# Optimization experiments

Measured on AMD Instinct MI355X. Metric: run time of the kernel, lower is better.

The kernel has to match this reference:

```python
import jax, jax.numpy as jnp
import numpy as np

N_ROWS = 5000  # hard-coded loop bound in the source
N_FEAT = 20    # hard-coded x size in the source


def setup_inputs() -> dict:
    key = jax.random.key(0)
    kA, kb, kx = jax.random.split(key, 3)
    A = jax.random.normal(kA, (N_ROWS, N_FEAT), dtype=jnp.float32)
    b = jax.random.normal(kb, (N_ROWS,), dtype=jnp.float32)
    # nn.Parameter initialized as uniform(low=1, high=13, size=20)
    x = 1.0 + 12.0 * jax.random.uniform(kx, (N_FEAT,), dtype=jnp.float32)
    return {"A": A, "b": b, "x": x}


def reference(A, b, x):
    # Original: loss = sum_i ||A[i,:] @ x - b||^2, where the scalar A[i]@x
    # broadcasts against the full vector b each iteration.
    # Vectorized: s = A @ x (shape [N_ROWS]); residual r[i,j] = s[i] - b[j].
    s = A @ x                                   # [5000]
    r = s[:, None] - b[None, :]                  # [5000, 5000] broadcasted residual
    return jnp.sum(r * r)
```

## Files before the change

kernel.cpp:

```cpp
#include <hip/hip_runtime.h>
#include <hip/hip_bf16.h>


#define N_ROWS 5000
#define N_FEAT 20
#define NBLK   20
#define BLKSZ  256

__device__ __forceinline__ double wave_reduce_sum(double v) {
    #pragma unroll
    for (int off = 32; off > 0; off >>= 1)
        v += __shfl_down(v, off, 64);
    return v;
}

__global__ __launch_bounds__(BLKSZ) void lsq_partial_kernel(
        const float* __restrict__ A, const float* __restrict__ b,
        const float* __restrict__ x, double* __restrict__ ws) {
    __shared__ float xs[N_FEAT];
    if (threadIdx.x < N_FEAT) xs[threadIdx.x] = x[threadIdx.x];
    __syncthreads();

    double s1 = 0.0, s2 = 0.0, b1 = 0.0, b2 = 0.0;
    for (int i = blockIdx.x * BLKSZ + threadIdx.x; i < N_ROWS;
         i += NBLK * BLKSZ) {
        const float* __restrict__ row = A + (long)i * N_FEAT;
        float s = 0.0f;
        #pragma unroll
        for (int k = 0; k < N_FEAT; ++k) s += row[k] * xs[k];
        s1 += (double)s;
        s2 += (double)s * (double)s;
        float bv = b[i];
        b1 += (double)bv;
        b2 += (double)bv * (double)bv;
    }

    s1 = wave_reduce_sum(s1);
    s2 = wave_reduce_sum(s2);
    b1 = wave_reduce_sum(b1);
    b2 = wave_reduce_sum(b2);

    __shared__ double red[4][4];
    int lane = threadIdx.x & 63;
    int wave = threadIdx.x >> 6;
    if (lane == 0) {
        red[wave][0] = s1; red[wave][1] = s2;
        red[wave][2] = b1; red[wave][3] = b2;
    }
    __syncthreads();
    if (threadIdx.x == 0) {
        double t0 = 0, t1 = 0, t2 = 0, t3 = 0;
        #pragma unroll
        for (int w = 0; w < 4; ++w) {
            t0 += red[w][0]; t1 += red[w][1];
            t2 += red[w][2]; t3 += red[w][3];
        }
        double* p = ws + 4 * blockIdx.x;
        p[0] = t0; p[1] = t1; p[2] = t2; p[3] = t3;
    }
}

__global__ __launch_bounds__(64) void lsq_finalize_kernel(
        const double* __restrict__ ws, float* __restrict__ out) {
    double s1 = 0, s2 = 0, b1 = 0, b2 = 0;
    if (threadIdx.x < NBLK) {
        const double* p = ws + 4 * threadIdx.x;
        s1 = p[0]; s2 = p[1]; b1 = p[2]; b2 = p[3];
    }
    s1 = wave_reduce_sum(s1);
    s2 = wave_reduce_sum(s2);
    b1 = wave_reduce_sum(b1);
    b2 = wave_reduce_sum(b2);
    if (threadIdx.x == 0) {
        double n = (double)N_ROWS;
        out[0] = (float)(n * s2 - 2.0 * s1 * b1 + n * b2);
    }
}

extern "C" void kernel_launch(void* const* d_in, const int* in_sizes, int n_in,
                              void* d_out, int out_size, void* d_ws, size_t ws_size,
                              hipStream_t stream) {
    const float* A = (const float*)d_in[0];
    const float* b = (const float*)d_in[1];
    const float* x = (const float*)d_in[2];
    float* out = (float*)d_out;
    double* ws = (double*)d_ws;

    lsq_partial_kernel<<<NBLK, BLKSZ, 0, stream>>>(A, b, x, ws);
    lsq_finalize_kernel<<<1, 64, 0, stream>>>(ws, out);
}
```

Before: 59.74 us.

## Fuse partial and finalize reductions into one single-block kernel with float4 loads

Replaces the two-kernel reduction (20 blocks plus a finalize launch) with one 1024-thread block that computes the row dot products, reduces them, and writes the final scalar. Rows are read as five float4 loads and x is held in registers. This removes a kernel launch and the workspace round trip, but puts the whole 400KB read on a single CU, which may limit memory bandwidth.

```diff
diff --git a/kernel.cpp b/kernel.cpp
--- a/kernel.cpp
+++ b/kernel.cpp
@@ -4,8 +4,8 @@
 
 #define N_ROWS 5000
 #define N_FEAT 20
-#define NBLK   20
-#define BLKSZ  256
+#define BLKSZ  1024
+#define NWAVES (BLKSZ / 64)
 
 __device__ __forceinline__ double wave_reduce_sum(double v) {
     #pragma unroll
@@ -14,23 +14,32 @@
     return v;
 }
 
-__global__ __launch_bounds__(BLKSZ) void lsq_partial_kernel(
+__global__ __launch_bounds__(BLKSZ) void lsq_fused_kernel(
         const float* __restrict__ A, const float* __restrict__ b,
-        const float* __restrict__ x, double* __restrict__ ws) {
+        const float* __restrict__ x, float* __restrict__ out) {
     __shared__ float xs[N_FEAT];
     if (threadIdx.x < N_FEAT) xs[threadIdx.x] = x[threadIdx.x];
     __syncthreads();
 
+    float x0 = xs[0],  x1 = xs[1],  x2 = xs[2],  x3 = xs[3],  x4 = xs[4];
+    float x5 = xs[5],  x6 = xs[6],  x7 = xs[7],  x8 = xs[8],  x9 = xs[9];
+    float x10 = xs[10], x11 = xs[11], x12 = xs[12], x13 = xs[13], x14 = xs[14];
+    float x15 = xs[15], x16 = xs[16], x17 = xs[17], x18 = xs[18], x19 = xs[19];
+
     double s1 = 0.0, s2 = 0.0, b1 = 0.0, b2 = 0.0;
-    for (int i = blockIdx.x * BLKSZ + threadIdx.x; i < N_ROWS;
-         i += NBLK * BLKSZ) {
-        const float* __restrict__ row = A + (long)i * N_FEAT;
-        float s = 0.0f;
-        #pragma unroll
-        for (int k = 0; k < N_FEAT; ++k) s += row[k] * xs[k];
+    for (int i = threadIdx.x; i < N_ROWS; i += BLKSZ) {
+        const float4* __restrict__ row = (const float4*)(A + (long)i * N_FEAT);
+        float4 r0 = row[0], r1 = row[1], r2 = row[2], r3 = row[3], r4 = row[4];
+        float bv = b[i];
+
+        float s = r0.x * x0  + r0.y * x1  + r0.z * x2  + r0.w * x3
+                + r1.x * x4  + r1.y * x5  + r1.z * x6  + r1.w * x7
+                + r2.x * x8  + r2.y * x9  + r2.z * x10 + r2.w * x11
+                + r3.x * x12 + r3.y * x13 + r3.z * x14 + r3.w * x15
+                + r4.x * x16 + r4.y * x17 + r4.z * x18 + r4.w * x19;
+
         s1 += (double)s;
         s2 += (double)s * (double)s;
-        float bv = b[i];
         b1 += (double)bv;
         b2 += (double)bv * (double)bv;
     }
@@ -40,7 +49,7 @@
     b1 = wave_reduce_sum(b1);
     b2 = wave_reduce_sum(b2);
 
-    __shared__ double red[4][4];
+    __shared__ double red[NWAVES][4];
     int lane = threadIdx.x & 63;
     int wave = threadIdx.x >> 6;
     if (lane == 0) {
@@ -51,29 +60,12 @@
     if (threadIdx.x == 0) {
         double t0 = 0, t1 = 0, t2 = 0, t3 = 0;
         #pragma unroll
-        for (int w = 0; w < 4; ++w) {
+        for (int w = 0; w < NWAVES; ++w) {
             t0 += red[w][0]; t1 += red[w][1];
             t2 += red[w][2]; t3 += red[w][3];
         }
-        double* p = ws + 4 * blockIdx.x;
-        p[0] = t0; p[1] = t1; p[2] = t2; p[3] = t3;
-    }
-}
-
-__global__ __launch_bounds__(64) void lsq_finalize_kernel(
-        const double* __restrict__ ws, float* __restrict__ out) {
-    double s1 = 0, s2 = 0, b1 = 0, b2 = 0;
-    if (threadIdx.x < NBLK) {
-        const double* p = ws + 4 * threadIdx.x;
-        s1 = p[0]; s2 = p[1]; b1 = p[2]; b2 = p[3];
-    }
-    s1 = wave_reduce_sum(s1);
-    s2 = wave_reduce_sum(s2);
-    b1 = wave_reduce_sum(b1);
-    b2 = wave_reduce_sum(b2);
-    if (threadIdx.x == 0) {
         double n = (double)N_ROWS;
-        out[0] = (float)(n * s2 - 2.0 * s1 * b1 + n * b2);
+        out[0] = (float)(n * t1 - 2.0 * t0 * t2 + n * t3);
     }
 }
 
@@ -84,8 +76,7 @@
     const float* b = (const float*)d_in[1];
     const float* x = (const float*)d_in[2];
     float* out = (float*)d_out;
-    double* ws = (double*)d_ws;
+    (void)d_ws; (void)ws_size;
 
-    lsq_partial_kernel<<<NBLK, BLKSZ, 0, stream>>>(A, b, x, ws);
-    lsq_finalize_kernel<<<1, 64, 0, stream>>>(ws, out);
+    lsq_fused_kernel<<<1, BLKSZ, 0, stream>>>(A, b, x, out);
 }
```

Result: slower. 62.81 us (+5.1%).
